# Performance work log

Measured on AMD Instinct MI355X. Metric: run time of the kernel, lower is better.

Reference implementation:

```python
import jax, jax.numpy as jnp
import numpy as np

B, F_IN, F_OUT, D, K = 32, 64, 64, 512, 64


def setup_inputs() -> dict:
    key = jax.random.key(0)
    k1, k2, k3 = jax.random.split(key, 3)
    x = jax.random.normal(k1, (B, F_IN, D), dtype=jnp.float32)
    # Evaluated monomial-word operators: K matrices of size D x D
    word_ops = jax.random.normal(k2, (K, D, D), dtype=jnp.float32)
    # nn.init.uniform_ -> U[0,1)
    coeff = jax.random.uniform(k3, (F_OUT, F_IN, K), dtype=jnp.float32)
    return {"x": x, "word_ops": word_ops, "coeff": coeff}


def reference(x, word_ops, coeff):
    # Per sample in the torch code:
    #   evals[i, d, k] = (X @ W_k)[i, d] = sum_e X[i, e] * W[k, e, d]
    #   res = tensordot(coeff, evals, ([1, 2], [0, 2]))  -> [F_out, D]
    # Fully batched fused contraction (replaces the Python loop over batch):
    # evals: [B, F_in, D, K]
    evals = jnp.einsum('bie,ked->bidk', x, word_ops)
    # out: [B, F_out, D]
    out = jnp.einsum('oik,bidk->bod', coeff, evals)
    return out
```

## Files before the change

### kernel.cpp

```cpp
#include <hip/hip_runtime.h>


#define KK 32768

typedef __attribute__((ext_vector_type(8))) short bf16x8;
typedef __attribute__((ext_vector_type(4))) float f32x4;

__device__ __forceinline__ unsigned short f2bf(float f) {
  unsigned int u = __float_as_uint(f);
  return (unsigned short)((u + 0x7FFFu + ((u >> 16) & 1u)) >> 16);
}

__device__ __forceinline__ void gld16(void* lds, const void* g) {
  __builtin_amdgcn_global_load_lds((const __attribute__((address_space(1))) void*)g,
                                   (__attribute__((address_space(3))) void*)lds,
                                   16, 0, 0);
}

__global__ __launch_bounds__(256) void convW(const float* __restrict__ W,
                                             unsigned short* __restrict__ WbT) {
  __shared__ float tile[64][65];
  int bx = blockIdx.x;
  int k = bx >> 6, et = (bx >> 3) & 7, dt = bx & 7;
  int t = threadIdx.x;
  const float* src = W + ((size_t)k * 512 + (size_t)et * 64) * 512 + dt * 64;
  int rr = t >> 6, cc = t & 63;
#pragma unroll
  for (int p = 0; p < 16; p++) {
    int e = p * 4 + rr;
    tile[e][cc] = src[(size_t)e * 512 + cc];
  }
  __syncthreads();
  int dl = t >> 4, eg = t & 15;
#pragma unroll
  for (int p = 0; p < 4; p++) {
    int d = p * 16 + dl;
    ushort4 v;
    v.x = f2bf(tile[eg * 4 + 0][d]);
    v.y = f2bf(tile[eg * 4 + 1][d]);
    v.z = f2bf(tile[eg * 4 + 2][d]);
    v.w = f2bf(tile[eg * 4 + 3][d]);
    *(ushort4*)(WbT + (size_t)(dt * 64 + d) * KK + k * 512 + et * 64 + eg * 4) = v;
  }
}

__global__ __launch_bounds__(256) void convX(const float* __restrict__ x,
                                             unsigned short* __restrict__ xT) {
  __shared__ unsigned short lds[64 * 130];
  int bx = blockIdx.x;
  int b = bx >> 2, ec = bx & 3;
  int t = threadIdx.x;
  const float* src = x + (size_t)b * 32768 + ec * 128;
#pragma unroll
  for (int j = 0; j < 32; j++) {
    int idx = j * 256 + t;
    int i = idx >> 7, e = idx & 127;
    lds[i * 130 + e] = f2bf(src[(size_t)i * 512 + e]);
  }
  __syncthreads();
  unsigned short* dst = xT + (size_t)b * 32768 + ec * 128 * 64;
#pragma unroll
  for (int j = 0; j < 32; j++) {
    int idx = j * 256 + t;
    int e = idx >> 6, i = idx & 63;
    dst[idx] = lds[i * 130 + e];
  }
}

__global__ __launch_bounds__(256) void convC(const float* __restrict__ c,
                                             unsigned short* __restrict__ cb) {
  __shared__ unsigned short lds[64 * 66];
  int rb = blockIdx.x;
  int t = threadIdx.x;
  const float* src = c + (size_t)rb * 4096;
#pragma unroll
  for (int j = 0; j < 16; j++) {
    int idx = j * 256 + t;
    int r = idx >> 6, k = idx & 63;
    lds[r * 66 + k] = f2bf(src[idx]);
  }
  __syncthreads();
#pragma unroll
  for (int j = 0; j < 16; j++) {
    int idx = j * 256 + t;
    int k = idx >> 6, r = idx & 63;
    cb[(size_t)k * 4096 + rb * 64 + r] = lds[r * 66 + k];
  }
}

__global__ __launch_bounds__(256, 2) void tkern(const unsigned short* __restrict__ xT,
                                                const unsigned short* __restrict__ cb,
                                                unsigned short* __restrict__ Tb) {
  __shared__ unsigned short xe[128 * 64];
  __shared__ unsigned short ckb[2][64 * 64];
  __shared__ unsigned short ot[64 * 132];
  int bx = blockIdx.x;
  int eq = bx & 3, kq = (bx >> 2) & 15, b = bx >> 6;
  int t = threadIdx.x;
  {
    const unsigned short* gx = xT + (size_t)b * 32768 + (size_t)eq * 8192;
#pragma unroll
    for (int j = 0; j < 4; j++) {
      int idx = j * 256 + t;
      int e = idx >> 3, cg = (idx & 7) ^ (e & 7);
      gld16((char*)xe + idx * 16, gx + e * 64 + cg * 8);
    }
    const unsigned short* gc = cb + (size_t)(kq * 4) * 4096;
#pragma unroll
    for (int j = 0; j < 2; j++) {
      int idx = j * 256 + t;
      int o = idx >> 3, cg = (idx & 7) ^ (o & 7);
      gld16((char*)ckb[0] + idx * 16, gc + o * 64 + cg * 8);
    }
  }
  int wid = t >> 6, lane = t & 63, q = lane >> 4, l16 = lane & 15;
  size_t mbase = (size_t)(b * 64) * KK;
#pragma unroll 1
  for (int kj = 0; kj < 4; kj++) {
    int cur = kj & 1;
    __syncthreads();
    if (kj < 3) {
      const unsigned short* gc = cb + (size_t)(kq * 4 + kj + 1) * 4096;
#pragma unroll
      for (int j = 0; j < 2; j++) {
        int idx = j * 256 + t;
        int o = idx >> 3, cg = (idx & 7) ^ (o & 7);
        gld16((char*)ckb[cur ^ 1] + idx * 16, gc + o * 64 + cg * 8);
      }
    }
    const unsigned short* ck = ckb[cur];
    f32x4 acc[4][2] = {};
    bf16x8 af[4][2], bfr[2][2];
#pragma unroll
    for (int mf = 0; mf < 4; mf++)
#pragma unroll
      for (int ks2 = 0; ks2 < 2; ks2++) {
        int row = mf * 16 + l16;
        int s2 = (ks2 * 4 + q) ^ (row & 7);
        af[mf][ks2] = *(const bf16x8*)(ck + row * 64 + s2 * 8);
      }
#pragma unroll
    for (int nf = 0; nf < 2; nf++) {
      int e = wid * 32 + nf * 16 + l16;
#pragma unroll
      for (int ks2 = 0; ks2 < 2; ks2++) {
        int s2 = (ks2 * 4 + q) ^ (e & 7);
        bfr[nf][ks2] = *(const bf16x8*)(xe + e * 64 + s2 * 8);
      }
    }
#pragma unroll
    for (int mf = 0; mf < 4; mf++)
#pragma unroll
      for (int nf = 0; nf < 2; nf++)
#pragma unroll
        for (int ks2 = 0; ks2 < 2; ks2++)
          acc[mf][nf] = __builtin_amdgcn_mfma_f32_16x16x32_bf16(af[mf][ks2], bfr[nf][ks2],
                                                                acc[mf][nf], 0, 0, 0);
#pragma unroll
    for (int mf = 0; mf < 4; mf++)
#pragma unroll
      for (int nf = 0; nf < 2; nf++)
#pragma unroll
        for (int r = 0; r < 4; r++) {
          int o = mf * 16 + q * 4 + r;
          int e = wid * 32 + nf * 16 + l16;
          ot[o * 132 + e] = f2bf(acc[mf][nf][r]);
        }
    __syncthreads();
    unsigned short* gdst = Tb + mbase + (size_t)(kq * 4 + kj) * 512 + eq * 128;
#pragma unroll
    for (int j = 0; j < 8; j++) {
      int idx = j * 256 + t;
      int o = idx >> 5, c = idx & 31;
      *(ushort4*)(gdst + (size_t)o * KK + c * 4) = *(const ushort4*)(ot + o * 132 + c * 4);
    }
  }
}

__global__ __launch_bounds__(256, 4) void gemm_kern(const unsigned short* __restrict__ A,
                                                    const unsigned short* __restrict__ Bt,
                                                    float* __restrict__ out) {
  __shared__ unsigned short As[128 * 64];
  __shared__ unsigned short Bs[128 * 64];
  int bx = blockIdx.x;
  int ks = bx & 15, nt = (bx >> 4) & 3, mt = bx >> 6;
  int m0 = mt * 128, n0 = nt * 128, k0 = ks * 2048;
  int t = threadIdx.x;
  int wid = t >> 6, lane = t & 63, q = lane >> 4, l16 = lane & 15;
  int wm = (wid & 1) * 64, wn = (wid >> 1) * 64;
  f32x4 acc[4][4] = {};
  int srow = t >> 3;
  int cg = (t & 7) ^ (srow & 7);
  const char* gabase = (const char*)(A + (size_t)m0 * KK + k0) + (size_t)srow * 65536 + cg * 16;
  const char* gbbase = (const char*)(Bt + (size_t)n0 * KK + k0) + (size_t)srow * 65536 + cg * 16;
  int sw0 = q ^ (l16 & 7);
  int sw1 = (4 | q) ^ (l16 & 7);
#pragma unroll 1
  for (int kc = 0; kc < 2048; kc += 64) {
    const char* ga = gabase + (size_t)kc * 2;
    const char* gb = gbbase + (size_t)kc * 2;
#pragma unroll
    for (int j = 0; j < 4; j++) {
      gld16((char*)As + (j * 256 + t) * 16, ga + (size_t)j * 32 * 65536);
      gld16((char*)Bs + (j * 256 + t) * 16, gb + (size_t)j * 32 * 65536);
    }
    __syncthreads();
#pragma unroll
    for (int ks2 = 0; ks2 < 2; ks2++) {
      int slot = ks2 ? sw1 : sw0;
      bf16x8 af[4], bfr[4];
#pragma unroll
      for (int fr = 0; fr < 4; fr++)
        af[fr] = *(const bf16x8*)(As + (wm + fr * 16 + l16) * 64 + slot * 8);
#pragma unroll
      for (int fc = 0; fc < 4; fc++)
        bfr[fc] = *(const bf16x8*)(Bs + (wn + fc * 16 + l16) * 64 + slot * 8);
#pragma unroll
      for (int fr = 0; fr < 4; fr++)
#pragma unroll
        for (int fc = 0; fc < 4; fc++)
          acc[fr][fc] = __builtin_amdgcn_mfma_f32_16x16x32_bf16(af[fr], bfr[fc], acc[fr][fc], 0, 0, 0);
    }
    __syncthreads();
  }
#pragma unroll
  for (int fr = 0; fr < 4; fr++)
#pragma unroll
    for (int fc = 0; fc < 4; fc++)
#pragma unroll
      for (int r = 0; r < 4; r++)
        atomicAdd(&out[(size_t)(m0 + wm + fr * 16 + q * 4 + r) * 512 + n0 + wn + fc * 16 + l16],
                  acc[fr][fc][r]);
}

__global__ __launch_bounds__(256) void fallback_kern(const float* __restrict__ x,
                                                     const float* __restrict__ W,
                                                     const float* __restrict__ coeff,
                                                     float* __restrict__ out) {
  __shared__ float ev[64][129];
  int b = blockIdx.x >> 6, k = blockIdx.x & 63;
  int t = threadIdx.x, dl = t & 127, half = t >> 7;
  const float* xb = x + (size_t)b * 64 * 512;
  const float* Wk = W + (size_t)k * 512 * 512;
  for (int dc = 0; dc < 4; dc++) {
    int d = dc * 128 + dl;
    for (int i = half * 32; i < half * 32 + 32; i++) {
      float acc = 0.f;
      const float* xr = xb + (size_t)i * 512;
#pragma unroll 4
      for (int e = 0; e < 512; e++) acc += xr[e] * Wk[(size_t)e * 512 + d];
      ev[i][dl] = acc;
    }
    __syncthreads();
    for (int o = half * 32; o < half * 32 + 32; o++) {
      float s = 0.f;
#pragma unroll 8
      for (int i = 0; i < 64; i++) s += coeff[((size_t)o * 64 + i) * 64 + k] * ev[i][dl];
      atomicAdd(&out[((size_t)(b * 64 + o)) * 512 + d], s);
    }
    __syncthreads();
  }
}

extern "C" void kernel_launch(void* const* d_in, const int* in_sizes, int n_in,
                              void* d_out, int out_size, void* d_ws, size_t ws_size,
                              hipStream_t stream) {
  const float* x = (const float*)d_in[0];
  const float* W = (const float*)d_in[1];
  const float* coeff = (const float*)d_in[2];
  float* out = (float*)d_out;
  const size_t OFF_XT = 33554432;
  const size_t OFF_CB = OFF_XT + 2097152;
  const size_t OFF_TB = OFF_CB + 524288;
  const size_t NEED = OFF_TB + 134217728;

  hipMemsetAsync(d_out, 0, (size_t)out_size * sizeof(float), stream);
  if (ws_size >= NEED) {
    unsigned short* WbT = (unsigned short*)d_ws;
    unsigned short* xT  = (unsigned short*)((char*)d_ws + OFF_XT);
    unsigned short* cb  = (unsigned short*)((char*)d_ws + OFF_CB);
    unsigned short* Tb  = (unsigned short*)((char*)d_ws + OFF_TB);
    convX<<<128, 256, 0, stream>>>(x, xT);
    convC<<<64, 256, 0, stream>>>(coeff, cb);
    convW<<<4096, 256, 0, stream>>>(W, WbT);
    tkern<<<2048, 256, 0, stream>>>(xT, cb, Tb);
    gemm_kern<<<1024, 256, 0, stream>>>(Tb, WbT, out);
  } else {
    fallback_kern<<<2048, 256, 0, stream>>>(x, W, coeff, out);
  }
}
```

Before: 246.9 us.

## Restructure T kernel to write directly and enlarge GEMM M tile to 256

The T-producing kernel now loads all four coefficient slices into LDS up front. It swaps the MFMA operand roles so each lane holds four contiguous K-columns, and stores bf16 results straight to global memory. This removes the LDS staging tile and the per-iteration barriers. The GEMM kernel doubles its M tile to 256 rows with 8x4 fragments per wave, which halves the grid and cuts B-tile reloads and atomics per output. The trade-off is more registers and LDS per block, so occupancy drops to 2 blocks per CU, and the T stores become narrower, less coalesced 8-byte writes.

```diff
diff --git a/kernel.cpp b/kernel.cpp
--- a/kernel.cpp
+++ b/kernel.cpp
@@ -88,12 +88,11 @@
   }
 }
 
-__global__ __launch_bounds__(256, 2) void tkern(const unsigned short* __restrict__ xT,
+__global__ __launch_bounds__(256, 3) void tkern(const unsigned short* __restrict__ xT,
                                                 const unsigned short* __restrict__ cb,
                                                 unsigned short* __restrict__ Tb) {
   __shared__ unsigned short xe[128 * 64];
-  __shared__ unsigned short ckb[2][64 * 64];
-  __shared__ unsigned short ot[64 * 132];
+  __shared__ unsigned short ck[4 * 64 * 64];
   int bx = blockIdx.x;
   int eq = bx & 3, kq = (bx >> 2) & 15, b = bx >> 6;
   int t = threadIdx.x;
@@ -107,88 +106,73 @@
     }
     const unsigned short* gc = cb + (size_t)(kq * 4) * 4096;
 #pragma unroll
-    for (int j = 0; j < 2; j++) {
-      int idx = j * 256 + t;
-      int o = idx >> 3, cg = (idx & 7) ^ (o & 7);
-      gld16((char*)ckb[0] + idx * 16, gc + o * 64 + cg * 8);
-    }
-  }
-  int wid = t >> 6, lane = t & 63, q = lane >> 4, l16 = lane & 15;
-  size_t mbase = (size_t)(b * 64) * KK;
-#pragma unroll 1
-  for (int kj = 0; kj < 4; kj++) {
-    int cur = kj & 1;
-    __syncthreads();
-    if (kj < 3) {
-      const unsigned short* gc = cb + (size_t)(kq * 4 + kj + 1) * 4096;
-#pragma unroll
-      for (int j = 0; j < 2; j++) {
-        int idx = j * 256 + t;
-        int o = idx >> 3, cg = (idx & 7) ^ (o & 7);
-        gld16((char*)ckb[cur ^ 1] + idx * 16, gc + o * 64 + cg * 8);
-      }
-    }
-    const unsigned short* ck = ckb[cur];
-    f32x4 acc[4][2] = {};
-    bf16x8 af[4][2], bfr[2][2];
-#pragma unroll
-    for (int mf = 0; mf < 4; mf++)
-#pragma unroll
-      for (int ks2 = 0; ks2 < 2; ks2++) {
-        int row = mf * 16 + l16;
-        int s2 = (ks2 * 4 + q) ^ (row & 7);
-        af[mf][ks2] = *(const bf16x8*)(ck + row * 64 + s2 * 8);
-      }
-#pragma unroll
-    for (int nf = 0; nf < 2; nf++) {
-      int e = wid * 32 + nf * 16 + l16;
-#pragma unroll
-      for (int ks2 = 0; ks2 < 2; ks2++) {
-        int s2 = (ks2 * 4 + q) ^ (e & 7);
-        bfr[nf][ks2] = *(const bf16x8*)(xe + e * 64 + s2 * 8);
-      }
-    }
-#pragma unroll
-    for (int mf = 0; mf < 4; mf++)
-#pragma unroll
-      for (int nf = 0; nf < 2; nf++)
-#pragma unroll
-        for (int ks2 = 0; ks2 < 2; ks2++)
-          acc[mf][nf] = __builtin_amdgcn_mfma_f32_16x16x32_bf16(af[mf][ks2], bfr[nf][ks2],
-                                                                acc[mf][nf], 0, 0, 0);
-#pragma unroll
-    for (int mf = 0; mf < 4; mf++)
-#pragma unroll
-      for (int nf = 0; nf < 2; nf++)
-#pragma unroll
-        for (int r = 0; r < 4; r++) {
-          int o = mf * 16 + q * 4 + r;
-          int e = wid * 32 + nf * 16 + l16;
-          ot[o * 132 + e] = f2bf(acc[mf][nf][r]);
-        }
-    __syncthreads();
-    unsigned short* gdst = Tb + mbase + (size_t)(kq * 4 + kj) * 512 + eq * 128;
-#pragma unroll
     for (int j = 0; j < 8; j++) {
       int idx = j * 256 + t;
-      int o = idx >> 5, c = idx & 31;
-      *(ushort4*)(gdst + (size_t)o * KK + c * 4) = *(const ushort4*)(ot + o * 132 + c * 4);
-    }
-  }
-}
-
-__global__ __launch_bounds__(256, 4) void gemm_kern(const unsigned short* __restrict__ A,
+      int row = idx >> 3, cg = (idx & 7) ^ (row & 7);
+      gld16((char*)ck + idx * 16, gc + row * 64 + cg * 8);
+    }
+  }
+  __syncthreads();
+  int wid = t >> 6, lane = t & 63, q = lane >> 4, l16 = lane & 15;
+  bf16x8 ax[2][2];
+#pragma unroll
+  for (int ef = 0; ef < 2; ef++)
+#pragma unroll
+    for (int ks2 = 0; ks2 < 2; ks2++) {
+      int e = wid * 32 + ef * 16 + l16;
+      int s2 = (ks2 * 4 + q) ^ (e & 7);
+      ax[ef][ks2] = *(const bf16x8*)(xe + e * 64 + s2 * 8);
+    }
+  size_t mbase = (size_t)(b * 64);
+#pragma unroll
+  for (int kj = 0; kj < 4; kj++) {
+    const unsigned short* ckk = ck + kj * 4096;
+    bf16x8 bc[4][2];
+#pragma unroll
+    for (int of = 0; of < 4; of++)
+#pragma unroll
+      for (int ks2 = 0; ks2 < 2; ks2++) {
+        int o = of * 16 + l16;
+        int s2 = (ks2 * 4 + q) ^ (o & 7);
+        bc[of][ks2] = *(const bf16x8*)(ckk + o * 64 + s2 * 8);
+      }
+    f32x4 acc[2][4] = {};
+#pragma unroll
+    for (int ef = 0; ef < 2; ef++)
+#pragma unroll
+      for (int of = 0; of < 4; of++)
+#pragma unroll
+        for (int ks2 = 0; ks2 < 2; ks2++)
+          acc[ef][of] = __builtin_amdgcn_mfma_f32_16x16x32_bf16(ax[ef][ks2], bc[of][ks2],
+                                                                acc[ef][of], 0, 0, 0);
+    int kcol = (kq * 4 + kj) * 512 + eq * 128 + wid * 32 + q * 4;
+#pragma unroll
+    for (int ef = 0; ef < 2; ef++)
+#pragma unroll
+      for (int of = 0; of < 4; of++) {
+        ushort4 v;
+        v.x = f2bf(acc[ef][of][0]);
+        v.y = f2bf(acc[ef][of][1]);
+        v.z = f2bf(acc[ef][of][2]);
+        v.w = f2bf(acc[ef][of][3]);
+        *(ushort4*)(Tb + (mbase + of * 16 + l16) * (size_t)KK + kcol + ef * 16) = v;
+      }
+  }
+}
+
+__global__ __launch_bounds__(256, 2) void gemm_kern(const unsigned short* __restrict__ A,
                                                     const unsigned short* __restrict__ Bt,
                                                     float* __restrict__ out) {
-  __shared__ unsigned short As[128 * 64];
+  __shared__ unsigned short As[256 * 64];
   __shared__ unsigned short Bs[128 * 64];
   int bx = blockIdx.x;
-  int ks = bx & 15, nt = (bx >> 4) & 3, mt = bx >> 6;
-  int m0 = mt * 128, n0 = nt * 128, k0 = ks * 2048;
+  int kslo = bx & 7, nt = (bx >> 3) & 3, kshi = (bx >> 5) & 1, mt = bx >> 6;
+  int ks = kshi * 8 + kslo;
+  int m0 = mt * 256, n0 = nt * 128, k0 = ks * 2048;
   int t = threadIdx.x;
   int wid = t >> 6, lane = t & 63, q = lane >> 4, l16 = lane & 15;
-  int wm = (wid & 1) * 64, wn = (wid >> 1) * 64;
-  f32x4 acc[4][4] = {};
+  int wm = (wid & 1) * 128, wn = (wid >> 1) * 64;
+  f32x4 acc[8][4] = {};
   int srow = t >> 3;
   int cg = (t & 7) ^ (srow & 7);
   const char* gabase = (const char*)(A + (size_t)m0 * KK + k0) + (size_t)srow * 65536 + cg * 16;
@@ -200,37 +184,38 @@
     const char* ga = gabase + (size_t)kc * 2;
     const char* gb = gbbase + (size_t)kc * 2;
 #pragma unroll
-    for (int j = 0; j < 4; j++) {
+    for (int j = 0; j < 8; j++)
       gld16((char*)As + (j * 256 + t) * 16, ga + (size_t)j * 32 * 65536);
+#pragma unroll
+    for (int j = 0; j < 4; j++)
       gld16((char*)Bs + (j * 256 + t) * 16, gb + (size_t)j * 32 * 65536);
-    }
     __syncthreads();
 #pragma unroll
     for (int ks2 = 0; ks2 < 2; ks2++) {
       int slot = ks2 ? sw1 : sw0;
-      bf16x8 af[4], bfr[4];
-#pragma unroll
-      for (int fr = 0; fr < 4; fr++)
-        af[fr] = *(const bf16x8*)(As + (wm + fr * 16 + l16) * 64 + slot * 8);
-#pragma unroll
-      for (int fc = 0; fc < 4; fc++)
-        bfr[fc] = *(const bf16x8*)(Bs + (wn + fc * 16 + l16) * 64 + slot * 8);
-#pragma unroll
-      for (int fr = 0; fr < 4; fr++)
-#pragma unroll
-        for (int fc = 0; fc < 4; fc++)
-          acc[fr][fc] = __builtin_amdgcn_mfma_f32_16x16x32_bf16(af[fr], bfr[fc], acc[fr][fc], 0, 0, 0);
-    }
-    __syncthreads();
-  }
-#pragma unroll
-  for (int fr = 0; fr < 4; fr++)
-#pragma unroll
-    for (int fc = 0; fc < 4; fc++)
+      bf16x8 af[8], bfr[4];
+#pragma unroll
+      for (int mf = 0; mf < 8; mf++)
+        af[mf] = *(const bf16x8*)(As + (wm + mf * 16 + l16) * 64 + slot * 8);
+#pragma unroll
+      for (int nf = 0; nf < 4; nf++)
+        bfr[nf] = *(const bf16x8*)(Bs + (wn + nf * 16 + l16) * 64 + slot * 8);
+#pragma unroll
+      for (int mf = 0; mf < 8; mf++)
+#pragma unroll
+        for (int nf = 0; nf < 4; nf++)
+          acc[mf][nf] = __builtin_amdgcn_mfma_f32_16x16x32_bf16(af[mf], bfr[nf], acc[mf][nf], 0, 0, 0);
+    }
+    __syncthreads();
+  }
+#pragma unroll
+  for (int mf = 0; mf < 8; mf++)
+#pragma unroll
+    for (int nf = 0; nf < 4; nf++)
 #pragma unroll
       for (int r = 0; r < 4; r++)
-        atomicAdd(&out[(size_t)(m0 + wm + fr * 16 + q * 4 + r) * 512 + n0 + wn + fc * 16 + l16],
-                  acc[fr][fc][r]);
+        atomicAdd(&out[(size_t)(m0 + wm + mf * 16 + q * 4 + r) * 512 + n0 + wn + nf * 16 + l16],
+                  acc[mf][nf][r]);
 }
 
 __global__ __launch_bounds__(256) void fallback_kern(const float* __restrict__ x,
@@ -284,7 +269,7 @@
     convC<<<64, 256, 0, stream>>>(coeff, cb);
     convW<<<4096, 256, 0, stream>>>(W, WbT);
     tkern<<<2048, 256, 0, stream>>>(xT, cb, Tb);
-    gemm_kern<<<1024, 256, 0, stream>>>(Tb, WbT, out);
+    gemm_kern<<<512, 256, 0, stream>>>(Tb, WbT, out);
   } else {
     fallback_kern<<<2048, 256, 0, stream>>>(x, W, coeff, out);
   }
```

Result: slower. 257.8 us (+4.4%).
